# Kernel optimization log

Hardware: AMD Instinct MI355X
Metric: run time of the kernel (lower is better)

## Reference

```python
import jax, jax.numpy as jnp
import numpy as np

N_V, N_G, K, C_IN, DW, NB, E = 8192, 4096, 128, 128, 64, 4, 65536
SIGMA, CUT = 4.0, 8.0


def setup_inputs() -> dict:
    key = jax.random.key(0)
    ks = iter(jax.random.split(key, 64))
    s = 0.05
    def rn(shape):
        return jax.random.normal(next(ks), shape, dtype=jnp.float32) * s
    p = {}
    p['vertices'] = jax.random.uniform(next(ks), (N_V, 3), dtype=jnp.float32) * 30.0
    p['graph_pos'] = jax.random.uniform(next(ks), (N_G, 3), dtype=jnp.float32) * 30.0
    p['x_in'] = jax.random.normal(next(ks), (N_V, C_IN), dtype=jnp.float32)
    p['graph_x'] = jax.random.normal(next(ks), (N_G, C_IN), dtype=jnp.float32)
    p['mass'] = jax.random.uniform(next(ks), (N_V,), dtype=jnp.float32) + 0.5
    p['evals'] = jax.random.uniform(next(ks), (K,), dtype=jnp.float32) * 10.0
    p['evecs'] = jax.random.normal(next(ks), (N_V, K), dtype=jnp.float32) * 0.011
    p['gradX'] = jax.random.normal(next(ks), (N_V, N_V), dtype=jnp.float32) * 0.01
    p['gradY'] = jax.random.normal(next(ks), (N_V, N_V), dtype=jnp.float32) * 0.01
    p['graph_edge_index'] = jax.random.randint(next(ks), (2, E), 0, N_G)
    p['graph_edge_weight'] = jax.random.uniform(next(ks), (E,), dtype=jnp.float32)
    p['lin1_w'] = rn((C_IN, DW)); p['lin1_b'] = rn((DW,))
    p['lin2_w'] = rn((C_IN, DW)); p['lin2_b'] = rn((DW,))
    p['diff_time'] = jax.random.uniform(next(ks), (NB, DW), dtype=jnp.float32) * 0.5 + 0.01
    p['A_re'] = rn((NB, DW, DW)); p['A_im'] = rn((NB, DW, DW))
    p['mlp_w0'] = rn((NB, 3 * DW, DW)); p['mlp_b0'] = rn((NB, DW))
    p['mlp_w1'] = rn((NB, DW, DW)); p['mlp_b1'] = rn((NB, DW))
    p['mlp_w2'] = rn((NB, DW, DW)); p['mlp_b2'] = rn((NB, DW))
    p['gcn1_w'] = rn((NB, DW, DW)); p['gcn1_b'] = rn((NB, DW))
    p['gcn2_w'] = rn((NB, DW, DW)); p['gcn2_b'] = rn((NB, DW))
    p['gs_w'] = rn((NB, DW, DW)); p['gs_b'] = rn((NB, DW))
    p['sg_w'] = rn((NB, DW, DW)); p['sg_b'] = rn((NB, DW))
    return p


def _gcn_conv(x, src, dst, ew, W, b, n):
    # PyG GCNConv with self-loops (fill 1.0): D^-1/2 (A+I) D^-1/2 (x W) + b
    xw = x @ W
    deg = jnp.ones((n,), xw.dtype).at[dst].add(ew)
    dinv = 1.0 / jnp.sqrt(deg)
    norm = dinv[src] * ew * dinv[dst]
    agg = jnp.zeros_like(xw).at[dst].add(norm[:, None] * xw[src])
    return agg + xw / deg[:, None] + b


def _forward(vertices, graph_pos, x_in, graph_x, mass, evals, evecs, gradX, gradY,
             graph_edge_weight, lin1_w, lin1_b, lin2_w, lin2_b, diff_time, A_re, A_im,
             mlp_w0, mlp_b0, mlp_w1, mlp_b1, mlp_w2, mlp_b2,
             gcn1_w, gcn1_b, gcn2_w, gcn2_b, gs_w, gs_b, sg_w, sg_b, graph_edge_index):
    n_v = vertices.shape[0]
    # torch.cdist + cutoff + exp(-d/sigma), under no_grad in the original
    d = jnp.sqrt(jnp.maximum(jnp.sum((vertices[:, None, :] - graph_pos[None, :, :]) ** 2, -1), 0.0))
    Wb = jax.lax.stop_gradient(jnp.where(d < CUT, jnp.exp(-d / SIGMA), 0.0))  # [n_v, n_g]
    deg_v = 1.0 + Wb.sum(1)  # vertex in-degree incl. self-loop (graphsurf direction)
    deg_g = 1.0 + Wb.sum(0)  # graph-node in-degree incl. self-loop (surfgraph direction)
    rsv = 1.0 / jnp.sqrt(deg_v)
    rsg = 1.0 / jnp.sqrt(deg_g)
    src, dst = graph_edge_index[0], graph_edge_index[1]
    diff_x = x_in @ lin1_w + lin1_b
    gx = graph_x @ lin2_w + lin2_b
    n_g = gx.shape[0]
    for i in range(NB):
        # --- DiffusionNet block (spectral) ---
        t = jnp.maximum(diff_time[i], 1e-8)
        spec = evecs.T @ (diff_x * mass[:, None])              # [K, DW]
        xd = evecs @ (jnp.exp(-evals[:, None] * t[None, :]) * spec)
        gX = gradX @ xd                                         # real part of gradient
        gY = gradY @ xd                                         # imag part of gradient
        br = gX @ A_re[i] - gY @ A_im[i]
        bi = gY @ A_re[i] + gX @ A_im[i]
        gf = jnp.tanh(gX * br + gY * bi)                        # spatial gradient features
        h = jnp.concatenate([diff_x, xd, gf], axis=-1)
        h = jax.nn.relu(h @ mlp_w0[i] + mlp_b0[i])
        h = jax.nn.relu(h @ mlp_w1[i] + mlp_b1[i])
        diff_x = diff_x + h @ mlp_w2[i] + mlp_b2[i]
        # --- internal graph GCN (eval mode: dropout = identity) ---
        gx = jax.nn.relu(_gcn_conv(gx, src, dst, graph_edge_weight, gcn1_w[i], gcn1_b[i], n_g))
        gx = _gcn_conv(gx, src, dst, graph_edge_weight, gcn2_w[i], gcn2_b[i], n_g)
        # --- bipartite GCNConvs on concatenated nodes ---
        xall = jnp.concatenate([diff_x, gx], axis=0)
        xw = xall @ gs_w[i]   # graphsurf: graph -> surface edges
        os_v = xw[:n_v] / deg_v[:, None] + (Wb @ xw[n_v:]) * rsv[:, None] + gs_b[i]
        os_g = xw[n_v:] + gs_b[i]
        xw2 = xall @ sg_w[i]  # surfgraph: surface -> graph edges
        og_g = xw2[n_v:] / deg_g[:, None] + (Wb.T @ xw2[:n_v]) * rsg[:, None] + sg_b[i]
        og_v = xw2[:n_v] + sg_b[i]
        diff_x = 0.5 * (os_v + og_v)
        gx = 0.5 * (os_g + og_g)
    return diff_x  # [n_v, C_out]


def reference(vertices, graph_pos, x_in, graph_x, mass, evals, evecs, gradX, gradY,
              graph_edge_index, graph_edge_weight, lin1_w, lin1_b, lin2_w, lin2_b,
              diff_time, A_re, A_im, mlp_w0, mlp_b0, mlp_w1, mlp_b1, mlp_w2, mlp_b2,
              gcn1_w, gcn1_b, gcn2_w, gcn2_b, gs_w, gs_b, sg_w, sg_b):
    return _forward(vertices, graph_pos, x_in, graph_x, mass, evals, evecs, gradX, gradY,
                    graph_edge_weight, lin1_w, lin1_b, lin2_w, lin2_b, diff_time, A_re, A_im,
                    mlp_w0, mlp_b0, mlp_w1, mlp_b1, mlp_w2, mlp_b2,
                    gcn1_w, gcn1_b, gcn2_w, gcn2_b, gs_w, gs_b, sg_w, sg_b, graph_edge_index)
```

## Files before the change

kernel.cpp:

```cpp
#include <hip/hip_runtime.h>
#include <hip/hip_bf16.h>

typedef unsigned short u16;
typedef __attribute__((ext_vector_type(8))) short sh8;
typedef __attribute__((ext_vector_type(4))) float f32x4;

#define NV 8192
#define NG 4096
#define NE 65536
#define NSLICE 32

__device__ __forceinline__ u16 f2bf(float f) {
  __hip_bfloat16 h = __float2bfloat16(f);
  return __builtin_bit_cast(u16, h);
}

__device__ __forceinline__ void gl_lds16(const void* g, void* l) {
  __builtin_amdgcn_global_load_lds(
      (const __attribute__((address_space(1))) void*)g,
      (__attribute__((address_space(3))) void*)l, 16, 0, 0);
}

__global__ void k_fill4(float* __restrict__ deg_v, float* __restrict__ deg_g,
                        float* __restrict__ deg_e, int* __restrict__ cnt) {
  int i = blockIdx.x * 256 + threadIdx.x;
  if (i < NV) deg_v[i] = 1.f;
  int j = i - NV;
  if (j >= 0 && j < NG) deg_g[j] = 1.f;
  j -= NG;
  if (j >= 0 && j < NG) deg_e[j] = 1.f;
  j -= NG;
  if (j >= 0 && j < NG) cnt[j] = 0;
}

__global__ __launch_bounds__(256) void k_wb_build(
    const float* __restrict__ vert, const float* __restrict__ gpos,
    u16* __restrict__ Wb, u16* __restrict__ WbT,
    float* __restrict__ deg_v, float* __restrict__ deg_g) {
  __shared__ float lv[192], lg[192], colp[256];
  __shared__ float tile[64][65];
  int t = threadIdx.x;
  int v0 = blockIdx.x * 64, g0 = blockIdx.y * 64;
  if (t < 192) { lv[t] = vert[(size_t)v0 * 3 + t]; lg[t] = gpos[(size_t)g0 * 3 + t]; }
  __syncthreads();
  int w = t >> 6, lane = t & 63;
  float gx_ = lg[lane * 3], gy_ = lg[lane * 3 + 1], gz_ = lg[lane * 3 + 2];
  float csum = 0.f;
  #pragma unroll 4
  for (int s = 0; s < 16; s++) {
    int vl = w + 4 * s;
    float dx = lv[vl * 3] - gx_, dy = lv[vl * 3 + 1] - gy_, dz = lv[vl * 3 + 2] - gz_;
    float d = sqrtf(dx * dx + dy * dy + dz * dz);
    float W = (d < 8.0f) ? expf(d * -0.25f) : 0.f;
    Wb[(size_t)(v0 + vl) * NG + g0 + lane] = f2bf(W);
    tile[vl][lane] = W;
    csum += W;
  }
  colp[t] = csum;
  __syncthreads();
  int r = t >> 2, q = t & 3;
  float rs = 0.f;
  #pragma unroll
  for (int j = 0; j < 16; j++) rs += tile[r][q * 16 + j];
  rs += __shfl_xor(rs, 1);
  rs += __shfl_xor(rs, 2);
  if (q == 0) atomicAdd(&deg_v[v0 + r], rs);
  if (w == 0) {
    float tot = colp[lane] + colp[64 + lane] + colp[128 + lane] + colp[192 + lane];
    atomicAdd(&deg_g[g0 + lane], tot);
  }
  if (WbT != nullptr) {
    #pragma unroll
    for (int j = 0; j < 2; j++) {
      int idx = j * 256 + t;
      int g = idx >> 3, v8 = (idx & 7) * 8;
      u16 pk[8];
      #pragma unroll
      for (int qq = 0; qq < 8; qq++) pk[qq] = f2bf(tile[v8 + qq][g]);
      *(uint4*)&WbT[(size_t)(g0 + g) * NV + v0 + v8] = *(uint4*)pk;
    }
  }
}

__global__ void k_recips(const float* __restrict__ deg_v, float* __restrict__ inv_v,
                         float* __restrict__ rs_v, const float* __restrict__ deg_g,
                         float* __restrict__ inv_g, float* __restrict__ rs_g,
                         const float* __restrict__ deg_e, float* __restrict__ inv_e,
                         float* __restrict__ rs_e) {
  int i = blockIdx.x * 256 + threadIdx.x;
  if (i < NV) { float d = deg_v[i]; inv_v[i] = 1.f / d; rs_v[i] = 1.f / sqrtf(d); }
  else if (i < NV + NG) {
    int j = i - NV; float d = deg_g[j]; inv_g[j] = 1.f / d; rs_g[j] = 1.f / sqrtf(d);
  } else if (i < NV + 2 * NG) {
    int j = i - NV - NG; float d = deg_e[j]; inv_e[j] = 1.f / d; rs_e[j] = 1.f / sqrtf(d);
  }
}

__global__ void k_edge_prep(const int* __restrict__ eidx, const float* __restrict__ ew,
                            float* __restrict__ deg_e, int* __restrict__ cnt) {
  int e = blockIdx.x * 256 + threadIdx.x;
  if (e < NE) { int d = eidx[NE + e]; atomicAdd(&deg_e[d], ew[e]); atomicAdd(&cnt[d], 1); }
}

__global__ __launch_bounds__(1024) void k_scan(const int* __restrict__ cnt,
    int* __restrict__ row_ptr, int* __restrict__ cursor) {
  __shared__ int buf0[1024], buf1[1024];
  int t = threadIdx.x;
  int b = t * 4;
  int c0 = cnt[b], c1 = cnt[b + 1], c2 = cnt[b + 2], c3 = cnt[b + 3];
  int s = c0 + c1 + c2 + c3;
  buf0[t] = s;
  __syncthreads();
  int* src = buf0; int* dst = buf1;
  for (int off = 1; off < 1024; off <<= 1) {
    int v = src[t];
    if (t >= off) v += src[t - off];
    dst[t] = v;
    __syncthreads();
    int* tmp = src; src = dst; dst = tmp;
  }
  int excl = (t == 0) ? 0 : src[t - 1];
  int r0 = excl, r1 = excl + c0, r2 = excl + c0 + c1, r3 = excl + c0 + c1 + c2;
  row_ptr[b] = r0; row_ptr[b + 1] = r1; row_ptr[b + 2] = r2; row_ptr[b + 3] = r3;
  cursor[b] = r0; cursor[b + 1] = r1; cursor[b + 2] = r2; cursor[b + 3] = r3;
  if (t == 1023) row_ptr[4096] = src[1023];
}

__global__ void k_scatter(const int* __restrict__ eidx, const float* __restrict__ ew,
                          const float* __restrict__ dinv, int* __restrict__ cursor,
                          int* __restrict__ csrc, float* __restrict__ cnorm) {
  int e = blockIdx.x * 256 + threadIdx.x;
  if (e < NE) {
    int s = eidx[e], d = eidx[NE + e];
    int slot = atomicAdd(&cursor[d], 1);
    csrc[slot] = s;
    cnorm[slot] = dinv[s] * ew[e] * dinv[d];
  }
}

__global__ __launch_bounds__(256) void k_evecsT(const float* __restrict__ ev, u16* __restrict__ evT) {
  __shared__ float tile[32][33];
  int t = threadIdx.x;
  int v0 = blockIdx.x * 32, k0 = blockIdx.y * 32;
  int r = t >> 3, c4 = (t & 7) * 4;
  float4 x = *(const float4*)(ev + (size_t)(v0 + r) * 128 + k0 + c4);
  tile[r][c4] = x.x; tile[r][c4 + 1] = x.y; tile[r][c4 + 2] = x.z; tile[r][c4 + 3] = x.w;
  __syncthreads();
  u16* dst = evT + (size_t)(k0 + r) * NV + v0 + c4;
  dst[0] = f2bf(tile[c4][r]); dst[1] = f2bf(tile[c4 + 1][r]);
  dst[2] = f2bf(tile[c4 + 2][r]); dst[3] = f2bf(tile[c4 + 3][r]);
}

__global__ __launch_bounds__(256) void gemm_setup(
    const float* __restrict__ gXm, const float* __restrict__ gYm,
    const u16* __restrict__ evT, float* __restrict__ parts,
    int nzHalf, int kchunk) {
  __shared__ __align__(16) char smem[49152];
  const int t = threadIdx.x;
  const int lane = t & 63, wave = t >> 6;
  const int m0 = blockIdx.x * 128;
  int kz = blockIdx.z;
  const float* A = gXm;
  if (kz >= nzHalf) { A = gYm; kz -= nzHalf; }
  const int kbeg = kz * kchunk;
  const int nt = kchunk >> 5;
  const int wm = (wave >> 1) * 64, wn = (wave & 1) * 64;
  const int arl = lane >> 3, asl = lane & 7;
  const int brl = lane >> 2, bsl = lane & 3;

  f32x4 acc[4][4];
  #pragma unroll
  for (int a = 0; a < 4; a++)
    #pragma unroll
    for (int b = 0; b < 4; b++) acc[a][b] = f32x4{0.f, 0.f, 0.f, 0.f};

  auto STAGE = [&](int buf, int k0) {
    char* base = smem + buf * 24576;
    #pragma unroll
    for (int j = 0; j < 4; j++) {
      int R0 = (wave * 4 + j) * 8;
      int r = R0 + arl;
      int gs = asl ^ (r & 7);
      gl_lds16(A + (size_t)(m0 + r) * NV + k0 + gs * 4, base + R0 * 128);
    }
    char* bb = base + 16384;
    #pragma unroll
    for (int j = 0; j < 2; j++) {
      int R0 = (wave * 2 + j) * 16;
      int r = R0 + brl;
      int gs = bsl ^ (r & 3);
      gl_lds16(evT + (size_t)r * NV + k0 + gs * 8, bb + R0 * 64);
    }
  };

  auto COMPUTE = [&](int buf) {
    char* base = smem + buf * 24576;
    const float* Af = (const float*)base;
    const u16* Bf = (const u16*)(base + 16384);
    sh8 av[4], bv[4];
    #pragma unroll
    for (int mf = 0; mf < 4; mf++) {
      int r = wm + mf * 16 + (lane & 15);
      int b2 = (lane >> 4) * 2;
      float4 f0 = *(const float4*)(Af + r * 32 + ((b2) ^ (r & 7)) * 4);
      float4 f1 = *(const float4*)(Af + r * 32 + ((b2 + 1) ^ (r & 7)) * 4);
      sh8 v;
      v[0] = (short)f2bf(f0.x); v[1] = (short)f2bf(f0.y);
      v[2] = (short)f2bf(f0.z); v[3] = (short)f2bf(f0.w);
      v[4] = (short)f2bf(f1.x); v[5] = (short)f2bf(f1.y);
      v[6] = (short)f2bf(f1.z); v[7] = (short)f2bf(f1.w);
      av[mf] = v;
    }
    #pragma unroll
    for (int nf = 0; nf < 4; nf++) {
      int r = wn + nf * 16 + (lane & 15);
      int s = (lane >> 4) ^ (r & 3);
      bv[nf] = *(const sh8*)(Bf + r * 32 + s * 8);
    }
    #pragma unroll
    for (int mf = 0; mf < 4; mf++)
      #pragma unroll
      for (int nf = 0; nf < 4; nf++)
        acc[mf][nf] = __builtin_amdgcn_mfma_f32_16x16x32_bf16(av[mf], bv[nf], acc[mf][nf], 0, 0, 0);
  };

  STAGE(0, kbeg);
  if (nt > 1) STAGE(1, kbeg + 32);
  for (int ti = 0; ti < nt; ti++) {
    if (ti + 1 < nt) { asm volatile("s_waitcnt vmcnt(6)" ::: "memory"); }
    else             { asm volatile("s_waitcnt vmcnt(0)" ::: "memory"); }
    __builtin_amdgcn_sched_barrier(0);
    __builtin_amdgcn_s_barrier();
    COMPUTE(ti & 1);
    __builtin_amdgcn_sched_barrier(0);
    __builtin_amdgcn_s_barrier();
    if (ti + 2 < nt) STAGE(ti & 1, kbeg + (ti + 2) * 32);
  }

  float* C = parts + (size_t)blockIdx.z * (NV * 128);
  #pragma unroll
  for (int mf = 0; mf < 4; mf++)
    #pragma unroll
    for (int nf = 0; nf < 4; nf++) {
      int row = m0 + wm + mf * 16 + (lane >> 4) * 4;
      int col = wn + nf * 16 + (lane & 15);
      #pragma unroll
      for (int q = 0; q < 4; q++)
        C[(size_t)(row + q) * 128 + col] = acc[mf][nf][q];
    }
}

__global__ __launch_bounds__(256) void gemm_bf16(
    const u16* __restrict__ Ab, int lda, const u16* __restrict__ BT, int ldbt,
    float* __restrict__ parts, int M, int kchunk) {
  __shared__ __align__(16) char smem[49152];
  const int t = threadIdx.x;
  const int lane = t & 63, wave = t >> 6;
  const int m0 = blockIdx.x * 128;
  const int kbeg = blockIdx.z * kchunk;
  const int nt = kchunk >> 6;
  const int wm = (wave >> 1) * 64, wn = (wave & 1) * 32;
  const int arl = lane >> 3, asl = lane & 7;

  f32x4 acc[4][2];
  #pragma unroll
  for (int a = 0; a < 4; a++)
    #pragma unroll
    for (int b = 0; b < 2; b++) acc[a][b] = f32x4{0.f, 0.f, 0.f, 0.f};

  auto STAGE = [&](int buf, int k0) {
    char* base = smem + buf * 24576;
    #pragma unroll
    for (int j = 0; j < 4; j++) {
      int R0 = (wave * 4 + j) * 8;
      int r = R0 + arl;
      int gs = asl ^ (r & 7);
      gl_lds16(Ab + (size_t)(m0 + r) * lda + k0 + gs * 8, base + R0 * 128);
    }
    char* bb = base + 16384;
    #pragma unroll
    for (int j = 0; j < 2; j++) {
      int R0 = (wave * 2 + j) * 8;
      int r = R0 + arl;
      int gs = asl ^ (r & 7);
      gl_lds16(BT + (size_t)r * ldbt + k0 + gs * 8, bb + R0 * 128);
    }
  };

  auto COMPUTE = [&](int buf) {
    char* base = smem + buf * 24576;
    const u16* Af = (const u16*)base;
    const u16* Bf = (const u16*)(base + 16384);
    #pragma unroll
    for (int kk = 0; kk < 2; kk++) {
      sh8 av[4], bv[2];
      #pragma unroll
      for (int mf = 0; mf < 4; mf++) {
        int r = wm + mf * 16 + (lane & 15);
        int g = kk * 4 + (lane >> 4);
        av[mf] = *(const sh8*)(Af + r * 64 + (g ^ (r & 7)) * 8);
      }
      #pragma unroll
      for (int nf = 0; nf < 2; nf++) {
        int r = wn + nf * 16 + (lane & 15);
        int g = kk * 4 + (lane >> 4);
        bv[nf] = *(const sh8*)(Bf + r * 64 + (g ^ (r & 7)) * 8);
      }
      #pragma unroll
      for (int mf = 0; mf < 4; mf++)
        #pragma unroll
        for (int nf = 0; nf < 2; nf++)
          acc[mf][nf] = __builtin_amdgcn_mfma_f32_16x16x32_bf16(av[mf], bv[nf], acc[mf][nf], 0, 0, 0);
    }
  };

  STAGE(0, kbeg);
  if (nt > 1) STAGE(1, kbeg + 64);
  for (int ti = 0; ti < nt; ti++) {
    if (ti + 1 < nt) { asm volatile("s_waitcnt vmcnt(6)" ::: "memory"); }
    else             { asm volatile("s_waitcnt vmcnt(0)" ::: "memory"); }
    __builtin_amdgcn_sched_barrier(0);
    __builtin_amdgcn_s_barrier();
    COMPUTE(ti & 1);
    __builtin_amdgcn_sched_barrier(0);
    __builtin_amdgcn_s_barrier();
    if (ti + 2 < nt) STAGE(ti & 1, kbeg + (ti + 2) * 64);
  }

  float* C = parts + (size_t)blockIdx.z * M * 64;
  #pragma unroll
  for (int mf = 0; mf < 4; mf++)
    #pragma unroll
    for (int nf = 0; nf < 2; nf++) {
      int row = m0 + wm + mf * 16 + (lane >> 4) * 4;
      int col = wn + nf * 16 + (lane & 15);
      #pragma unroll
      for (int q = 0; q < 4; q++)
        C[(size_t)(row + q) * 64 + col] = acc[mf][nf][q];
    }
}

template<int BN, bool AF32, bool ATRANS>
__global__ __launch_bounds__(256) void gemm_k(
    const void* __restrict__ Aptr, const void* __restrict__ A2, int zsplit2,
    const u16* __restrict__ BT, float* __restrict__ Cpart,
    int M, int N, int lda, int ldbt, int kchunk) {
  constexpr int NF = BN / 32;
  __shared__ u16 lA[128 * 40];
  __shared__ u16 lB[BN * 40];
  const int t = threadIdx.x;
  const int m0 = blockIdx.x * 128, n0 = blockIdx.y * BN;
  const void* Ause = Aptr;
  int kz = blockIdx.z;
  if (A2 != nullptr && kz >= zsplit2) { Ause = A2; kz -= zsplit2; }
  const int kbeg = kz * kchunk;
  const int lane = t & 63, wave = t >> 6;
  const int wm = (wave >> 1) * 64, wn = (wave & 1) * (BN / 2);
  f32x4 zero = {0.f, 0.f, 0.f, 0.f};
  f32x4 acc[4][NF];
  #pragma unroll
  for (int a = 0; a < 4; a++)
    #pragma unroll
    for (int b = 0; b < NF; b++) acc[a][b] = zero;

  for (int k0 = kbeg; k0 < kbeg + kchunk; k0 += 32) {
    if constexpr (!ATRANS) {
      const int r = t >> 1, cc = (t & 1) * 16;
      const u16* A = (const u16*)Ause + (size_t)(m0 + r) * lda + k0 + cc;
      *(uint4*)&lA[r * 40 + cc] = *(const uint4*)A;
      *(uint4*)&lA[r * 40 + cc + 8] = *(const uint4*)(A + 8);
    } else {
      const int kl = t >> 3, mb = (t & 7) * 16;
      const u16* A = (const u16*)Ause + (size_t)(k0 + kl) * lda + m0 + mb;
      u16 vals[16];
      *(uint4*)&vals[0] = *(const uint4*)A;
      *(uint4*)&vals[8] = *(const uint4*)(A + 8);
      #pragma unroll
      for (int j = 0; j < 16; j++) lA[(mb + j) * 40 + kl] = vals[j];
    }
    if constexpr (BN == 64) {
      const int r = t >> 2, cc = (t & 3) * 8;
      const u16* B = BT + (size_t)(n0 + r) * ldbt + k0 + cc;
      *(uint4*)&lB[r * 40 + cc] = *(const uint4*)B;
    } else {
      const int r = t >> 1, cc = (t & 1) * 16;
      const u16* B = BT + (size_t)(n0 + r) * ldbt + k0 + cc;
      *(uint4*)&lB[r * 40 + cc] = *(const uint4*)B;
      *(uint4*)&lB[r * 40 + cc + 8] = *(const uint4*)(B + 8);
    }
    __syncthreads();
    sh8 af[4], bfv[NF];
    #pragma unroll
    for (int mf = 0; mf < 4; mf++)
      af[mf] = *(const sh8*)&lA[(wm + mf * 16 + (lane & 15)) * 40 + (lane >> 4) * 8];
    #pragma unroll
    for (int nf = 0; nf < NF; nf++)
      bfv[nf] = *(const sh8*)&lB[(wn + nf * 16 + (lane & 15)) * 40 + (lane >> 4) * 8];
    #pragma unroll
    for (int mf = 0; mf < 4; mf++)
      #pragma unroll
      for (int nf = 0; nf < NF; nf++)
        acc[mf][nf] = __builtin_amdgcn_mfma_f32_16x16x32_bf16(af[mf], bfv[nf], acc[mf][nf], 0, 0, 0);
    __syncthreads();
  }
  float* C = Cpart + (size_t)blockIdx.z * M * N;
  #pragma unroll
  for (int mf = 0; mf < 4; mf++)
    #pragma unroll
    for (int nf = 0; nf < NF; nf++) {
      const int row = m0 + wm + mf * 16 + (lane >> 4) * 4;
      const int col = n0 + wn + nf * 16 + (lane & 15);
      #pragma unroll
      for (int q = 0; q < 4; q++)
        C[(size_t)(row + q) * N + col] = acc[mf][nf][q];
    }
}

__global__ void k_reduce(const float* __restrict__ parts, float* __restrict__ dst, int len, int nz) {
  int i = (blockIdx.x * 256 + threadIdx.x) * 4;
  if (i >= len) return;
  float4 s = *(const float4*)(parts + i);
  for (int z = 1; z < nz; z++) {
    float4 v = *(const float4*)(parts + (size_t)z * len + i);
    s.x += v.x; s.y += v.y; s.z += v.z; s.w += v.w;
  }
  *(float4*)(dst + i) = s;
}

__global__ void k_reduce2(const float* __restrict__ parts, float* __restrict__ dst, int len, int nz) {
  int i = (blockIdx.x * 256 + threadIdx.x) * 4;
  if (i >= 2 * len) return;
  int mat = i / len, j = i - mat * len;
  const float* src = parts + (size_t)mat * nz * len + j;
  float4 s = *(const float4*)src;
  for (int z = 1; z < nz; z++) {
    float4 v = *(const float4*)(src + (size_t)z * len);
    s.x += v.x; s.y += v.y; s.z += v.z; s.w += v.w;
  }
  *(float4*)(dst + i) = s;
}

__global__ __launch_bounds__(256) void k_lin_both(const float* __restrict__ x_in,
    const float* __restrict__ graph_x, const float* __restrict__ W1,
    const float* __restrict__ b1, const float* __restrict__ W2,
    const float* __restrict__ b2, float* __restrict__ outV, float* __restrict__ outG) {
  __shared__ float lW[8192];
  __shared__ float lb[64];
  int bb = blockIdx.x;
  bool isV = bb < 2048;
  const float* W = isV ? W1 : W2;
  const float* bi = isV ? b1 : b2;
  const float* A = isV ? x_in : graph_x;
  float* out = isV ? outV : outG;
  int rb = isV ? bb : bb - 2048;
  int t = threadIdx.x;
  for (int i = t; i < 8192; i += 256) lW[i] = W[i];
  if (t < 64) lb[t] = bi[t];
  __syncthreads();
  int row = rb * 4 + (t >> 6), c = t & 63;
  const float* Ar = A + (size_t)row * 128;
  float acc = lb[c];
  #pragma unroll 8
  for (int k = 0; k < 128; k++) acc += Ar[k] * lW[k * 64 + c];
  out[(size_t)row * 64 + c] = acc;
}

__global__ __launch_bounds__(64) void k_spec_part(const float* __restrict__ evecs,
    const float* __restrict__ mass, const float* __restrict__ dx, float* __restrict__ sp) {
  int k = blockIdx.x, c = threadIdx.x;
  int v0 = blockIdx.y * 256;
  float a0 = 0, a1 = 0, a2 = 0, a3 = 0;
  for (int v = v0; v < v0 + 256; v += 4) {
    a0 += evecs[(size_t)(v + 0) * 128 + k] * mass[v + 0] * dx[(size_t)(v + 0) * 64 + c];
    a1 += evecs[(size_t)(v + 1) * 128 + k] * mass[v + 1] * dx[(size_t)(v + 1) * 64 + c];
    a2 += evecs[(size_t)(v + 2) * 128 + k] * mass[v + 2] * dx[(size_t)(v + 2) * 64 + c];
    a3 += evecs[(size_t)(v + 3) * 128 + k] * mass[v + 3] * dx[(size_t)(v + 3) * 64 + c];
  }
  sp[(size_t)blockIdx.y * 8192 + k * 64 + c] = (a0 + a1) + (a2 + a3);
}

__global__ void k_es(const float* __restrict__ sp, const float* __restrict__ evals,
                     const float* __restrict__ dt, float* __restrict__ Es) {
  int i = blockIdx.x * 256 + threadIdx.x;
  int k = i >> 6, c = i & 63;
  float s = 0.f;
  #pragma unroll 8
  for (int z = 0; z < NSLICE; z++) s += sp[(size_t)z * 8192 + i];
  Es[i] = expf(-evals[k] * fmaxf(dt[c], 1e-8f)) * s;
}

__global__ __launch_bounds__(256) void k_xdgf(const float* __restrict__ evecs,
    const float* __restrict__ GXE, const float* __restrict__ GYE,
    const float* __restrict__ Es, const float* __restrict__ Are,
    const float* __restrict__ Aim, float* __restrict__ xd, float* __restrict__ gf) {
  __shared__ float lE[8192];
  __shared__ float lr[4096], li[4096];
  __shared__ float lgx[256], lgy[256];
  int t = threadIdx.x;
  for (int i = t; i < 8192; i += 256) lE[i] = Es[i];
  for (int i = t; i < 4096; i += 256) { lr[i] = Are[i]; li[i] = Aim[i]; }
  __syncthreads();
  int wr = t >> 6, c = t & 63;
  int row = blockIdx.x * 4 + wr;
  const float* er = evecs + (size_t)row * 128;
  const float* xr = GXE + (size_t)row * 128;
  const float* yr = GYE + (size_t)row * 128;
  float a0 = 0, a1 = 0, a2 = 0;
  #pragma unroll 8
  for (int k = 0; k < 128; k++) {
    float s = lE[k * 64 + c];
    a0 += er[k] * s; a1 += xr[k] * s; a2 += yr[k] * s;
  }
  lgx[wr * 64 + c] = a1;
  lgy[wr * 64 + c] = a2;
  __syncthreads();
  float br = 0.f, bi = 0.f;
  #pragma unroll 8
  for (int k = 0; k < 64; k++) {
    float gx = lgx[wr * 64 + k], gy = lgy[wr * 64 + k];
    float ar = lr[k * 64 + c], ai = li[k * 64 + c];
    br += gx * ar - gy * ai;
    bi += gy * ar + gx * ai;
  }
  xd[(size_t)row * 64 + c] = a0;
  gf[(size_t)row * 64 + c] = tanhf(a1 * br + a2 * bi);
}

__global__ __launch_bounds__(256) void k_mlp0(const float* __restrict__ dx,
    const float* __restrict__ xd, const float* __restrict__ gf,
    const float* __restrict__ W0, const float* __restrict__ b0, float* __restrict__ h1) {
  __shared__ float lW[12288];
  __shared__ float lb[64];
  int t = threadIdx.x;
  for (int i = t; i < 12288; i += 256) lW[i] = W0[i];
  if (t < 64) lb[t] = b0[t];
  __syncthreads();
  int row = blockIdx.x * 4 + (t >> 6), c = t & 63;
  const float* a0 = dx + (size_t)row * 64;
  const float* a1 = xd + (size_t)row * 64;
  const float* a2 = gf + (size_t)row * 64;
  float acc = lb[c];
  #pragma unroll 8
  for (int k = 0; k < 64; k++) acc += a0[k] * lW[k * 64 + c];
  #pragma unroll 8
  for (int k = 0; k < 64; k++) acc += a1[k] * lW[(64 + k) * 64 + c];
  #pragma unroll 8
  for (int k = 0; k < 64; k++) acc += a2[k] * lW[(128 + k) * 64 + c];
  h1[(size_t)row * 64 + c] = fmaxf(acc, 0.f);
}

__global__ __launch_bounds__(256) void k_mlp12(const float* __restrict__ h1,
    const float* __restrict__ W1, const float* __restrict__ b1,
    const float* __restrict__ W2, const float* __restrict__ b2, float* __restrict__ dx) {
  __shared__ float l1[4096], l2[4096], lb1[64], lb2[64], lrow[256];
  int t = threadIdx.x;
  for (int i = t; i < 4096; i += 256) { l1[i] = W1[i]; l2[i] = W2[i]; }
  if (t < 64) lb1[t] = b1[t];
  else if (t < 128) lb2[t - 64] = b2[t - 64];
  __syncthreads();
  int wr = t >> 6, c = t & 63;
  int row = blockIdx.x * 4 + wr;
  const float* hr = h1 + (size_t)row * 64;
  float h2 = lb1[c];
  #pragma unroll 8
  for (int k = 0; k < 64; k++) h2 += hr[k] * l1[k * 64 + c];
  h2 = fmaxf(h2, 0.f);
  lrow[wr * 64 + c] = h2;
  __syncthreads();
  float o = lb2[c] + dx[(size_t)row * 64 + c];
  #pragma unroll 8
  for (int k = 0; k < 64; k++) o += lrow[wr * 64 + k] * l2[k * 64 + c];
  dx[(size_t)row * 64 + c] = o;
}

template<bool BIAS, bool RELU, bool RES>
__global__ __launch_bounds__(256) void k_mm64(const float* __restrict__ A,
    const float* __restrict__ W, const float* __restrict__ b,
    const float* __restrict__ res, float* __restrict__ out) {
  __shared__ float lW[4096];
  __shared__ float lb[64];
  int t = threadIdx.x;
  for (int i = t; i < 4096; i += 256) lW[i] = W[i];
  if constexpr (BIAS) { if (t < 64) lb[t] = b[t]; }
  __syncthreads();
  int row = blockIdx.x * 4 + (t >> 6), c = t & 63;
  const float* Ar = A + (size_t)row * 64;
  float acc = 0.f;
  #pragma unroll 8
  for (int k = 0; k < 64; k++) acc += Ar[k] * lW[k * 64 + c];
  if constexpr (BIAS) acc += lb[c];
  if constexpr (RES) acc += res[(size_t)row * 64 + c];
  if constexpr (RELU) acc = fmaxf(acc, 0.f);
  out[(size_t)row * 64 + c] = acc;
}

template<bool TP, bool TQ>
__global__ __launch_bounds__(256) void k_mm_dual(const float* __restrict__ A,
    const float* __restrict__ W1, const float* __restrict__ W2,
    float* __restrict__ P, float* __restrict__ Q,
    u16* __restrict__ PT, u16* __restrict__ QT, int R) {
  __shared__ float l1[4096], l2[4096];
  int t = threadIdx.x;
  for (int i = t; i < 4096; i += 256) { l1[i] = W1[i]; l2[i] = W2[i]; }
  __syncthreads();
  int row = blockIdx.x * 4 + (t >> 6), c = t & 63;
  const float* Ar = A + (size_t)row * 64;
  float p = 0.f, q = 0.f;
  #pragma unroll 8
  for (int k = 0; k < 64; k++) { float a = Ar[k]; p += a * l1[k * 64 + c]; q += a * l2[k * 64 + c]; }
  P[(size_t)row * 64 + c] = p;
  Q[(size_t)row * 64 + c] = q;
  if constexpr (TP) PT[(size_t)c * R + row] = f2bf(p);
  if constexpr (TQ) QT[(size_t)c * R + row] = f2bf(q);
}

__global__ __launch_bounds__(64) void k_aggmm(const float* __restrict__ xw,
    const int* __restrict__ rp, const int* __restrict__ csrc,
    const float* __restrict__ cnorm, const float* __restrict__ invdeg,
    const float* __restrict__ b1, const float* __restrict__ W2, float* __restrict__ out) {
  __shared__ float lrow[64];
  int g = blockIdx.x, c = threadIdx.x;
  float acc = xw[(size_t)g * 64 + c] * invdeg[g] + b1[c];
  int j1 = rp[g + 1];
  for (int j = rp[g]; j < j1; j++) acc += cnorm[j] * xw[(size_t)csrc[j] * 64 + c];
  acc = fmaxf(acc, 0.f);
  lrow[c] = acc;
  __syncthreads();
  float o = 0.f;
  #pragma unroll 8
  for (int k = 0; k < 64; k++) o += lrow[k] * W2[k * 64 + c];
  out[(size_t)g * 64 + c] = o;
}

__global__ __launch_bounds__(64) void k_aggdual(const float* __restrict__ xw,
    const int* __restrict__ rp, const int* __restrict__ csrc,
    const float* __restrict__ cnorm, const float* __restrict__ invdeg,
    const float* __restrict__ b2, const float* __restrict__ gsw,
    const float* __restrict__ sgw, float* __restrict__ xw_g,
    float* __restrict__ xw2_g, u16* __restrict__ xwgT) {
  __shared__ float lrow[64];
  int g = blockIdx.x, c = threadIdx.x;
  float acc = xw[(size_t)g * 64 + c] * invdeg[g] + b2[c];
  int j1 = rp[g + 1];
  for (int j = rp[g]; j < j1; j++) acc += cnorm[j] * xw[(size_t)csrc[j] * 64 + c];
  lrow[c] = acc;
  __syncthreads();
  float p = 0.f, q = 0.f;
  #pragma unroll 8
  for (int k = 0; k < 64; k++) {
    float r = lrow[k];
    p += r * gsw[k * 64 + c];
    q += r * sgw[k * 64 + c];
  }
  xw_g[(size_t)g * 64 + c] = p;
  xw2_g[(size_t)g * 64 + c] = q;
  xwgT[(size_t)c * NG + g] = f2bf(p);
}

__global__ void k_combine(const float* __restrict__ xw_v, const float* __restrict__ Wbp,
    const float* __restrict__ xw2_v, const float* __restrict__ xw_g,
    const float* __restrict__ WbTp, const float* __restrict__ xw2_g,
    const float* __restrict__ inv_deg_v, const float* __restrict__ rsv,
    const float* __restrict__ inv_deg_g, const float* __restrict__ rsg,
    const float* __restrict__ gsb, const float* __restrict__ sgb,
    float* __restrict__ dx, float* __restrict__ gx) {
  int idx = blockIdx.x * 256 + threadIdx.x;
  if (idx < NV * 64) {
    int v = idx >> 6, c = idx & 63;
    dx[idx] = 0.5f * (xw_v[idx] * inv_deg_v[v] + Wbp[idx] * rsv[v] + gsb[c] + xw2_v[idx] + sgb[c]);
  } else {
    int j = idx - NV * 64;
    int g = j >> 6, c = j & 63;
    gx[j] = 0.5f * (xw_g[j] + gsb[c] + xw2_g[j] * inv_deg_g[g] + WbTp[j] * rsg[g] + sgb[c]);
  }
}

extern "C" void kernel_launch(void* const* d_in, const int* in_sizes, int n_in,
                              void* d_out, int out_size, void* d_ws, size_t ws_size,
                              hipStream_t stream) {
  const float* vertices  = (const float*)d_in[0];
  const float* graph_pos = (const float*)d_in[1];
  const float* x_in      = (const float*)d_in[2];
  const float* graph_x   = (const float*)d_in[3];
  const float* mass      = (const float*)d_in[4];
  const float* evals     = (const float*)d_in[5];
  const float* evecs     = (const float*)d_in[6];
  const float* gradX     = (const float*)d_in[7];
  const float* gradY     = (const float*)d_in[8];
  const int*   eidx      = (const int*)d_in[9];
  const float* ew        = (const float*)d_in[10];
  const float* lin1_w    = (const float*)d_in[11];
  const float* lin1_b    = (const float*)d_in[12];
  const float* lin2_w    = (const float*)d_in[13];
  const float* lin2_b    = (const float*)d_in[14];
  const float* diff_time = (const float*)d_in[15];
  const float* A_re      = (const float*)d_in[16];
  const float* A_im      = (const float*)d_in[17];
  const float* mlp_w0    = (const float*)d_in[18];
  const float* mlp_b0    = (const float*)d_in[19];
  const float* mlp_w1    = (const float*)d_in[20];
  const float* mlp_b1    = (const float*)d_in[21];
  const float* mlp_w2    = (const float*)d_in[22];
  const float* mlp_b2    = (const float*)d_in[23];
  const float* gcn1_w    = (const float*)d_in[24];
  const float* gcn1_b    = (const float*)d_in[25];
  const float* gcn2_w    = (const float*)d_in[26];
  const float* gcn2_b    = (const float*)d_in[27];
  const float* gs_w      = (const float*)d_in[28];
  const float* gs_b      = (const float*)d_in[29];
  const float* sg_w      = (const float*)d_in[30];
  const float* sg_b      = (const float*)d_in[31];

  char* base = (char*)d_ws;
  size_t off = 0;
  auto alloc = [&](size_t nbytes) -> void* {
    void* p = base + off;
    off += (nbytes + 255) & ~(size_t)255;
    return p;
  };
  const size_t MBy = 1024 * 1024;
  u16*   Wb_bf   = (u16*)alloc((size_t)NV * NG * 2);
  u16*   evecsT  = (u16*)alloc((size_t)128 * NV * 2);
  float* GXE2    = (float*)alloc((size_t)2 * NV * 128 * 4);
  float* GXE     = GXE2;
  float* GYE     = GXE2 + (size_t)NV * 128;
  float* sp      = (float*)alloc((size_t)NSLICE * 8192 * 4);
  float* Es      = (float*)alloc(8192 * 4);
  float* diffx   = (float*)alloc((size_t)NV * 64 * 4);
  float* gxb     = (float*)alloc((size_t)NG * 64 * 4);
  float* xd      = (float*)alloc((size_t)NV * 64 * 4);
  float* gf      = (float*)alloc((size_t)NV * 64 * 4);
  float* h1      = (float*)alloc((size_t)NV * 64 * 4);
  float* xw_v    = (float*)alloc((size_t)NV * 64 * 4);
  float* xw2_v   = (float*)alloc((size_t)NV * 64 * 4);
  float* xw_g    = (float*)alloc((size_t)NG * 64 * 4);
  float* xw2_g   = (float*)alloc((size_t)NG * 64 * 4);
  float* xw1     = (float*)alloc((size_t)NG * 64 * 4);
  float* xw2k    = (float*)alloc((size_t)NG * 64 * 4);
  u16*   xwgT    = (u16*)alloc((size_t)64 * NG * 2);
  u16*   xw2vT   = (u16*)alloc((size_t)64 * NV * 2);
  float* Wbp     = (float*)alloc((size_t)NV * 64 * 4);
  float* WbTp    = (float*)alloc((size_t)NG * 64 * 4);
  float* deg_v   = (float*)alloc(NV * 4);
  float* inv_deg_v = (float*)alloc(NV * 4);
  float* rsv     = (float*)alloc(NV * 4);
  float* deg_g   = (float*)alloc(NG * 4);
  float* inv_deg_g = (float*)alloc(NG * 4);
  float* rsg     = (float*)alloc(NG * 4);
  float* deg_e   = (float*)alloc(NG * 4);
  float* invdeg_e = (float*)alloc(NG * 4);
  float* dinv_e  = (float*)alloc(NG * 4);
  int*   cnt     = (int*)alloc(NG * 4);
  int*   row_ptr = (int*)alloc((NG + 1) * 4);
  int*   cursor  = (int*)alloc(NG * 4);
  int*   csr_src = (int*)alloc(NE * 4);
  float* csr_norm = (float*)alloc(NE * 4);

  size_t avail = ws_size > off ? ws_size - off : 0;
  u16* WbT_bf = nullptr;
  int nzHalf;
  size_t partsBytes;
  if (avail >= 129 * MBy)      { WbT_bf = (u16*)alloc((size_t)NG * NV * 2); partsBytes = 64 * MBy; nzHalf = 8; }
  else if (avail >= 97 * MBy)  { WbT_bf = (u16*)alloc((size_t)NG * NV * 2); partsBytes = 32 * MBy; nzHalf = 4; }
  else if (avail >= 81 * MBy)  { WbT_bf = (u16*)alloc((size_t)NG * NV * 2); partsBytes = 16 * MBy; nzHalf = 2; }
  else if (avail >= 33 * MBy)  { partsBytes = 32 * MBy; nzHalf = 4; }
  else                          { partsBytes = 16 * MBy; nzHalf = 2; }
  float* parts = (float*)alloc(partsBytes);
  if (off > ws_size) return;

  dim3 B256(256);

  k_fill4<<<dim3(80), B256, 0, stream>>>(deg_v, deg_g, deg_e, cnt);
  k_wb_build<<<dim3(128, 64), B256, 0, stream>>>(vertices, graph_pos, Wb_bf, WbT_bf, deg_v, deg_g);
  k_edge_prep<<<dim3(256), B256, 0, stream>>>(eidx, ew, deg_e, cnt);
  k_recips<<<dim3(64), B256, 0, stream>>>(deg_v, inv_deg_v, rsv, deg_g, inv_deg_g, rsg,
                                          deg_e, invdeg_e, dinv_e);
  k_scan<<<dim3(1), dim3(1024), 0, stream>>>(cnt, row_ptr, cursor);
  k_scatter<<<dim3(256), B256, 0, stream>>>(eidx, ew, dinv_e, cursor, csr_src, csr_norm);
  k_evecsT<<<dim3(256, 4), B256, 0, stream>>>(evecs, evecsT);
  gemm_setup<<<dim3(64, 1, 2 * nzHalf), B256, 0, stream>>>(
      gradX, gradY, evecsT, parts, nzHalf, 8192 / nzHalf);
  k_reduce2<<<dim3(2048), B256, 0, stream>>>(parts, GXE2, NV * 128, nzHalf);
  k_lin_both<<<dim3(3072), B256, 0, stream>>>(x_in, graph_x, lin1_w, lin1_b, lin2_w, lin2_b, diffx, gxb);

  for (int i = 0; i < 4; i++) {
    const float* dtrow = diff_time + i * 64;
    k_spec_part<<<dim3(128, NSLICE), dim3(64), 0, stream>>>(evecs, mass, diffx, sp);
    k_es<<<dim3(32), B256, 0, stream>>>(sp, evals, dtrow, Es);
    k_xdgf<<<dim3(2048), B256, 0, stream>>>(evecs, GXE, GYE, Es, A_re + i * 4096, A_im + i * 4096, xd, gf);
    k_mlp0<<<dim3(2048), B256, 0, stream>>>(diffx, xd, gf, mlp_w0 + i * 12288, mlp_b0 + i * 64, h1);
    k_mlp12<<<dim3(2048), B256, 0, stream>>>(h1, mlp_w1 + i * 4096, mlp_b1 + i * 64,
        mlp_w2 + i * 4096, mlp_b2 + i * 64, diffx);
    k_mm64<false, false, false><<<dim3(1024), B256, 0, stream>>>(gxb, gcn1_w + i * 4096, nullptr, nullptr, xw1);
    k_aggmm<<<dim3(NG), dim3(64), 0, stream>>>(xw1, row_ptr, csr_src, csr_norm, invdeg_e,
        gcn1_b + i * 64, gcn2_w + i * 4096, xw2k);
    k_aggdual<<<dim3(NG), dim3(64), 0, stream>>>(xw2k, row_ptr, csr_src, csr_norm, invdeg_e,
        gcn2_b + i * 64, gs_w + i * 4096, sg_w + i * 4096, xw_g, xw2_g, xwgT);
    k_mm_dual<false, true><<<dim3(2048), B256, 0, stream>>>(diffx, gs_w + i * 4096, sg_w + i * 4096,
        xw_v, xw2_v, nullptr, xw2vT, NV);
    gemm_bf16<<<dim3(64, 1, 8), B256, 0, stream>>>(
        Wb_bf, NG, xwgT, NG, parts, NV, 512);
    k_reduce<<<dim3(512), B256, 0, stream>>>(parts, Wbp, NV * 64, 8);
    if (WbT_bf != nullptr) {
      gemm_bf16<<<dim3(32, 1, 16), B256, 0, stream>>>(
          WbT_bf, NV, xw2vT, NV, parts, NG, 512);
    } else {
      gemm_k<64, false, true><<<dim3(32, 1, 16), B256, 0, stream>>>(
          Wb_bf, nullptr, 1 << 30, xw2vT, parts, NG, 64, NG, NV, 512);
    }
    k_reduce<<<dim3(256), B256, 0, stream>>>(parts, WbTp, NG * 64, 16);
    k_combine<<<dim3(3072), B256, 0, stream>>>(xw_v, Wbp, xw2_v, xw_g, WbTp, xw2_g,
        inv_deg_v, rsv, inv_deg_g, rsg, gs_b + i * 64, sg_b + i * 64, diffx, gxb);
  }

  hipMemcpyAsync(d_out, diffx, (size_t)NV * 64 * 4, hipMemcpyDeviceToDevice, stream);
}
```

Before: 1.152 ms.

## Store Wb in pre-swizzled tile panels and replace split-K setup GEMM

The kernel that builds Wb now writes it, and its transpose, as contiguous pre-swizzled 128x64 bf16 tiles. A new gemm_panel kernel streams each tile straight into LDS with fully contiguous loads, replacing the strided row-major loads in the per-block Wb GEMMs. The setup gradX/gradY times evecs GEMM is rewritten without split-K: 64-row blocks with a 128-wide K stage and 128KB of dynamic LDS write directly to the output, which removes the partials buffer and the k_reduce2 pass. The cost is a workspace requirement of about 146MB for the fast path, and the setup GEMM now runs with fewer blocks and higher LDS use per block, which can lower occupancy.

```diff
diff --git a/kernel.cpp b/kernel.cpp
--- a/kernel.cpp
+++ b/kernel.cpp
@@ -35,7 +35,7 @@
 
 __global__ __launch_bounds__(256) void k_wb_build(
     const float* __restrict__ vert, const float* __restrict__ gpos,
-    u16* __restrict__ Wb, u16* __restrict__ WbT,
+    u16* __restrict__ WbRow, u16* __restrict__ WbP, u16* __restrict__ WbTP,
     float* __restrict__ deg_v, float* __restrict__ deg_g) {
   __shared__ float lv[192], lg[192], colp[256];
   __shared__ float tile[64][65];
@@ -52,32 +52,47 @@
     float dx = lv[vl * 3] - gx_, dy = lv[vl * 3 + 1] - gy_, dz = lv[vl * 3 + 2] - gz_;
     float d = sqrtf(dx * dx + dy * dy + dz * dz);
     float W = (d < 8.0f) ? expf(d * -0.25f) : 0.f;
-    Wb[(size_t)(v0 + vl) * NG + g0 + lane] = f2bf(W);
+    if (WbRow != nullptr) WbRow[(size_t)(v0 + vl) * NG + g0 + lane] = f2bf(W);
     tile[vl][lane] = W;
     csum += W;
   }
   colp[t] = csum;
   __syncthreads();
-  int r = t >> 2, q = t & 3;
+  int r4 = t >> 2, q = t & 3;
   float rs = 0.f;
   #pragma unroll
-  for (int j = 0; j < 16; j++) rs += tile[r][q * 16 + j];
+  for (int j = 0; j < 16; j++) rs += tile[r4][q * 16 + j];
   rs += __shfl_xor(rs, 1);
   rs += __shfl_xor(rs, 2);
-  if (q == 0) atomicAdd(&deg_v[v0 + r], rs);
+  if (q == 0) atomicAdd(&deg_v[v0 + r4], rs);
   if (w == 0) {
     float tot = colp[lane] + colp[64 + lane] + colp[128 + lane] + colp[192 + lane];
     atomicAdd(&deg_g[g0 + lane], tot);
   }
-  if (WbT != nullptr) {
+  if (WbP != nullptr) {
+    size_t tb = ((size_t)(v0 >> 7) * 64 + (g0 >> 6)) * 8192;
     #pragma unroll
     for (int j = 0; j < 2; j++) {
       int idx = j * 256 + t;
-      int g = idx >> 3, v8 = (idx & 7) * 8;
+      int vr = idx >> 3, k8 = (idx & 7) * 8;
       u16 pk[8];
       #pragma unroll
-      for (int qq = 0; qq < 8; qq++) pk[qq] = f2bf(tile[v8 + qq][g]);
-      *(uint4*)&WbT[(size_t)(g0 + g) * NV + v0 + v8] = *(uint4*)pk;
+      for (int qq = 0; qq < 8; qq++) pk[qq] = f2bf(tile[vr][k8 + qq]);
+      int r = (v0 & 64) + vr;
+      *(uint4*)&WbP[tb + (size_t)r * 64 + (size_t)(((k8 >> 3) ^ (r & 7)) << 3)] = *(uint4*)pk;
+    }
+  }
+  if (WbTP != nullptr) {
+    size_t tb = ((size_t)(g0 >> 7) * 128 + (v0 >> 6)) * 8192;
+    #pragma unroll
+    for (int j = 0; j < 2; j++) {
+      int idx = j * 256 + t;
+      int gr = idx >> 3, v8 = (idx & 7) * 8;
+      u16 pk[8];
+      #pragma unroll
+      for (int qq = 0; qq < 8; qq++) pk[qq] = f2bf(tile[v8 + qq][gr]);
+      int r = (g0 & 64) + gr;
+      *(uint4*)&WbTP[tb + (size_t)r * 64 + (size_t)(((v8 >> 3) ^ (r & 7)) << 3)] = *(uint4*)pk;
     }
   }
 }
@@ -151,102 +166,185 @@
   dst[2] = f2bf(tile[c4 + 2][r]); dst[3] = f2bf(tile[c4 + 3][r]);
 }
 
-__global__ __launch_bounds__(256) void gemm_setup(
+__global__ __launch_bounds__(256) void gemm_setup2(
     const float* __restrict__ gXm, const float* __restrict__ gYm,
-    const u16* __restrict__ evT, float* __restrict__ parts,
-    int nzHalf, int kchunk) {
-  __shared__ __align__(16) char smem[49152];
+    const u16* __restrict__ evT, float* __restrict__ C2) {
+  extern __shared__ __align__(16) char smem[];
   const int t = threadIdx.x;
   const int lane = t & 63, wave = t >> 6;
-  const int m0 = blockIdx.x * 128;
-  int kz = blockIdx.z;
-  const float* A = gXm;
-  if (kz >= nzHalf) { A = gYm; kz -= nzHalf; }
-  const int kbeg = kz * kchunk;
-  const int nt = kchunk >> 5;
-  const int wm = (wave >> 1) * 64, wn = (wave & 1) * 64;
-  const int arl = lane >> 3, asl = lane & 7;
-  const int brl = lane >> 2, bsl = lane & 3;
-
-  f32x4 acc[4][4];
+  const int rl = lane & 15, hi = lane >> 4;
+  const int mat = blockIdx.x >> 7, mb = blockIdx.x & 127;
+  const int m0 = mb * 64;
+  const float* A = mat ? gYm : gXm;
+  const int wm = (wave >> 1) * 32, wn = (wave & 1) * 64;
+
+  f32x4 acc[2][4];
   #pragma unroll
-  for (int a = 0; a < 4; a++)
+  for (int a = 0; a < 2; a++)
     #pragma unroll
     for (int b = 0; b < 4; b++) acc[a][b] = f32x4{0.f, 0.f, 0.f, 0.f};
 
   auto STAGE = [&](int buf, int k0) {
-    char* base = smem + buf * 24576;
-    #pragma unroll
-    for (int j = 0; j < 4; j++) {
-      int R0 = (wave * 4 + j) * 8;
-      int r = R0 + arl;
-      int gs = asl ^ (r & 7);
-      gl_lds16(A + (size_t)(m0 + r) * NV + k0 + gs * 4, base + R0 * 128);
-    }
-    char* bb = base + 16384;
-    #pragma unroll
-    for (int j = 0; j < 2; j++) {
-      int R0 = (wave * 2 + j) * 16;
-      int r = R0 + brl;
-      int gs = bsl ^ (r & 3);
-      gl_lds16(evT + (size_t)r * NV + k0 + gs * 8, bb + R0 * 64);
+    char* aB = smem + buf * 65536;
+    #pragma unroll
+    for (int jj = 0; jj < 8; jj++) {
+      int j = wave * 8 + jj;
+      int r = 2 * j + (lane >> 5);
+      const float* src = A + (size_t)(m0 + r) * NV + k0 + (((lane & 31) ^ (r & 7)) << 2);
+      gl_lds16(src, aB + j * 1024);
+    }
+    char* bB = aB + 32768;
+    #pragma unroll
+    for (int jj = 0; jj < 8; jj++) {
+      int j = wave * 8 + jj;
+      int n = 4 * j + (lane >> 4);
+      const u16* srcb = evT + (size_t)n * NV + k0 + (((lane & 15) ^ (n & 7)) << 3);
+      gl_lds16(srcb, bB + j * 1024);
     }
   };
 
   auto COMPUTE = [&](int buf) {
-    char* base = smem + buf * 24576;
-    const float* Af = (const float*)base;
-    const u16* Bf = (const u16*)(base + 16384);
-    sh8 av[4], bv[4];
-    #pragma unroll
-    for (int mf = 0; mf < 4; mf++) {
-      int r = wm + mf * 16 + (lane & 15);
-      int b2 = (lane >> 4) * 2;
-      float4 f0 = *(const float4*)(Af + r * 32 + ((b2) ^ (r & 7)) * 4);
-      float4 f1 = *(const float4*)(Af + r * 32 + ((b2 + 1) ^ (r & 7)) * 4);
-      sh8 v;
-      v[0] = (short)f2bf(f0.x); v[1] = (short)f2bf(f0.y);
-      v[2] = (short)f2bf(f0.z); v[3] = (short)f2bf(f0.w);
-      v[4] = (short)f2bf(f1.x); v[5] = (short)f2bf(f1.y);
-      v[6] = (short)f2bf(f1.z); v[7] = (short)f2bf(f1.w);
-      av[mf] = v;
-    }
-    #pragma unroll
-    for (int nf = 0; nf < 4; nf++) {
-      int r = wn + nf * 16 + (lane & 15);
-      int s = (lane >> 4) ^ (r & 3);
-      bv[nf] = *(const sh8*)(Bf + r * 32 + s * 8);
-    }
-    #pragma unroll
-    for (int mf = 0; mf < 4; mf++)
-      #pragma unroll
-      for (int nf = 0; nf < 4; nf++)
-        acc[mf][nf] = __builtin_amdgcn_mfma_f32_16x16x32_bf16(av[mf], bv[nf], acc[mf][nf], 0, 0, 0);
+    const float* Af = (const float*)(smem + buf * 65536);
+    const u16* Bf = (const u16*)(smem + buf * 65536 + 32768);
+    #pragma unroll
+    for (int step = 0; step < 4; step++) {
+      sh8 av[2], bv[4];
+      #pragma unroll
+      for (int mf = 0; mf < 2; mf++) {
+        int r = wm + mf * 16 + rl;
+        int s0 = step * 8 + hi * 2;
+        f32x4 lo = *(const f32x4*)(Af + r * 128 + ((s0 ^ (r & 7)) << 2));
+        f32x4 hi4 = *(const f32x4*)(Af + r * 128 + (((s0 + 1) ^ (r & 7)) << 2));
+        sh8 v;
+        v[0] = (short)f2bf(lo[0]); v[1] = (short)f2bf(lo[1]);
+        v[2] = (short)f2bf(lo[2]); v[3] = (short)f2bf(lo[3]);
+        v[4] = (short)f2bf(hi4[0]); v[5] = (short)f2bf(hi4[1]);
+        v[6] = (short)f2bf(hi4[2]); v[7] = (short)f2bf(hi4[3]);
+        av[mf] = v;
+      }
+      #pragma unroll
+      for (int nf = 0; nf < 4; nf++) {
+        int n = wn + nf * 16 + rl;
+        int s = step * 4 + hi;
+        bv[nf] = *(const sh8*)(Bf + n * 128 + ((s ^ (n & 7)) << 3));
+      }
+      #pragma unroll
+      for (int mf = 0; mf < 2; mf++)
+        #pragma unroll
+        for (int nf = 0; nf < 4; nf++)
+          acc[mf][nf] = __builtin_amdgcn_mfma_f32_16x16x32_bf16(av[mf], bv[nf], acc[mf][nf], 0, 0, 0);
+    }
   };
 
-  STAGE(0, kbeg);
-  if (nt > 1) STAGE(1, kbeg + 32);
-  for (int ti = 0; ti < nt; ti++) {
-    if (ti + 1 < nt) { asm volatile("s_waitcnt vmcnt(6)" ::: "memory"); }
+  STAGE(0, 0);
+  STAGE(1, 128);
+  for (int ti = 0; ti < 64; ti++) {
+    if (ti + 1 < 64) { asm volatile("s_waitcnt vmcnt(16)" ::: "memory"); }
     else             { asm volatile("s_waitcnt vmcnt(0)" ::: "memory"); }
     __builtin_amdgcn_sched_barrier(0);
     __builtin_amdgcn_s_barrier();
     COMPUTE(ti & 1);
     __builtin_amdgcn_sched_barrier(0);
     __builtin_amdgcn_s_barrier();
-    if (ti + 2 < nt) STAGE(ti & 1, kbeg + (ti + 2) * 32);
-  }
-
-  float* C = parts + (size_t)blockIdx.z * (NV * 128);
+    if (ti + 2 < 64) STAGE(ti & 1, (ti + 2) * 128);
+  }
+
+  float* C = C2 + (size_t)mat * NV * 128;
   #pragma unroll
-  for (int mf = 0; mf < 4; mf++)
+  for (int mf = 0; mf < 2; mf++)
     #pragma unroll
     for (int nf = 0; nf < 4; nf++) {
-      int row = m0 + wm + mf * 16 + (lane >> 4) * 4;
-      int col = wn + nf * 16 + (lane & 15);
+      int row = m0 + wm + mf * 16 + hi * 4;
+      int col = wn + nf * 16 + rl;
       #pragma unroll
       for (int q = 0; q < 4; q++)
         C[(size_t)(row + q) * 128 + col] = acc[mf][nf][q];
+    }
+}
+
+__global__ __launch_bounds__(256) void gemm_panel(
+    const u16* __restrict__ Apan, int KT, const u16* __restrict__ BT, int ldbt,
+    float* __restrict__ parts, int M, int nz, int ktpz) {
+  __shared__ __align__(16) char smem[49152];
+  const int t = threadIdx.x;
+  const int lane = t & 63, wave = t >> 6;
+  const int rl = lane & 15, hi = lane >> 4;
+  const int mb = blockIdx.x / nz, z = blockIdx.x % nz;
+  const int kt0 = z * ktpz;
+  const int wm = wave * 32;
+
+  f32x4 acc[2][4];
+  #pragma unroll
+  for (int a = 0; a < 2; a++)
+    #pragma unroll
+    for (int b = 0; b < 4; b++) acc[a][b] = f32x4{0.f, 0.f, 0.f, 0.f};
+
+  auto STAGE = [&](int buf, int kt) {
+    char* aB = smem + buf * 24576;
+    const u16* tbase = Apan + ((size_t)mb * KT + kt) * 8192;
+    #pragma unroll
+    for (int jj = 0; jj < 4; jj++) {
+      int j = wave * 4 + jj;
+      gl_lds16(tbase + j * 512 + lane * 8, aB + j * 1024);
+    }
+    char* bB = aB + 16384;
+    #pragma unroll
+    for (int jj = 0; jj < 2; jj++) {
+      int j = wave * 2 + jj;
+      int n = 8 * j + (lane >> 3);
+      const u16* srcb = BT + (size_t)n * ldbt + kt * 64 + (((lane & 7) ^ (n & 7)) << 3);
+      gl_lds16(srcb, bB + j * 1024);
+    }
+  };
+
+  auto COMPUTE = [&](int buf) {
+    const u16* Af = (const u16*)(smem + buf * 24576);
+    const u16* Bf = Af + 8192;
+    #pragma unroll
+    for (int step = 0; step < 2; step++) {
+      sh8 av[2], bv[4];
+      int s = step * 4 + hi;
+      #pragma unroll
+      for (int mf = 0; mf < 2; mf++) {
+        int r = wm + mf * 16 + rl;
+        av[mf] = *(const sh8*)(Af + r * 64 + ((s ^ (r & 7)) << 3));
+      }
+      #pragma unroll
+      for (int nf = 0; nf < 4; nf++) {
+        int n = nf * 16 + rl;
+        bv[nf] = *(const sh8*)(Bf + n * 64 + ((s ^ (n & 7)) << 3));
+      }
+      #pragma unroll
+      for (int mf = 0; mf < 2; mf++)
+        #pragma unroll
+        for (int nf = 0; nf < 4; nf++)
+          acc[mf][nf] = __builtin_amdgcn_mfma_f32_16x16x32_bf16(av[mf], bv[nf], acc[mf][nf], 0, 0, 0);
+    }
+  };
+
+  STAGE(0, kt0);
+  if (ktpz > 1) STAGE(1, kt0 + 1);
+  for (int ti = 0; ti < ktpz; ti++) {
+    if (ti + 1 < ktpz) { asm volatile("s_waitcnt vmcnt(6)" ::: "memory"); }
+    else               { asm volatile("s_waitcnt vmcnt(0)" ::: "memory"); }
+    __builtin_amdgcn_sched_barrier(0);
+    __builtin_amdgcn_s_barrier();
+    COMPUTE(ti & 1);
+    __builtin_amdgcn_sched_barrier(0);
+    __builtin_amdgcn_s_barrier();
+    if (ti + 2 < ktpz) STAGE(ti & 1, kt0 + ti + 2);
+  }
+
+  float* C = parts + (size_t)z * M * 64;
+  #pragma unroll
+  for (int mf = 0; mf < 2; mf++)
+    #pragma unroll
+    for (int nf = 0; nf < 4; nf++) {
+      int row = mb * 128 + wm + mf * 16 + hi * 4;
+      int col = nf * 16 + rl;
+      #pragma unroll
+      for (int q = 0; q < 4; q++)
+        C[(size_t)(row + q) * 64 + col] = acc[mf][nf][q];
     }
 }
 
@@ -422,19 +520,6 @@
   float4 s = *(const float4*)(parts + i);
   for (int z = 1; z < nz; z++) {
     float4 v = *(const float4*)(parts + (size_t)z * len + i);
-    s.x += v.x; s.y += v.y; s.z += v.z; s.w += v.w;
-  }
-  *(float4*)(dst + i) = s;
-}
-
-__global__ void k_reduce2(const float* __restrict__ parts, float* __restrict__ dst, int len, int nz) {
-  int i = (blockIdx.x * 256 + threadIdx.x) * 4;
-  if (i >= 2 * len) return;
-  int mat = i / len, j = i - mat * len;
-  const float* src = parts + (size_t)mat * nz * len + j;
-  float4 s = *(const float4*)src;
-  for (int z = 1; z < nz; z++) {
-    float4 v = *(const float4*)(src + (size_t)z * len);
     s.x += v.x; s.y += v.y; s.z += v.z; s.w += v.w;
   }
   *(float4*)(dst + i) = s;
@@ -719,7 +804,6 @@
     return p;
   };
   const size_t MBy = 1024 * 1024;
-  u16*   Wb_bf   = (u16*)alloc((size_t)NV * NG * 2);
   u16*   evecsT  = (u16*)alloc((size_t)128 * NV * 2);
   float* GXE2    = (float*)alloc((size_t)2 * NV * 128 * 4);
   float* GXE     = GXE2;
@@ -757,30 +841,32 @@
   float* csr_norm = (float*)alloc(NE * 4);
 
   size_t avail = ws_size > off ? ws_size - off : 0;
-  u16* WbT_bf = nullptr;
-  int nzHalf;
-  size_t partsBytes;
-  if (avail >= 129 * MBy)      { WbT_bf = (u16*)alloc((size_t)NG * NV * 2); partsBytes = 64 * MBy; nzHalf = 8; }
-  else if (avail >= 97 * MBy)  { WbT_bf = (u16*)alloc((size_t)NG * NV * 2); partsBytes = 32 * MBy; nzHalf = 4; }
-  else if (avail >= 81 * MBy)  { WbT_bf = (u16*)alloc((size_t)NG * NV * 2); partsBytes = 16 * MBy; nzHalf = 2; }
-  else if (avail >= 33 * MBy)  { partsBytes = 32 * MBy; nzHalf = 4; }
-  else                          { partsBytes = 16 * MBy; nzHalf = 2; }
-  float* parts = (float*)alloc(partsBytes);
+  u16 *WbP = nullptr, *WbTP = nullptr, *WbRow = nullptr;
+  float* parts;
+  if (avail >= 146 * MBy) {
+    WbP  = (u16*)alloc((size_t)NV * NG * 2);
+    WbTP = (u16*)alloc((size_t)NG * NV * 2);
+    parts = (float*)alloc(16 * MBy);
+  } else if (avail >= 81 * MBy) {
+    WbRow = (u16*)alloc((size_t)NV * NG * 2);
+    parts = (float*)alloc(16 * MBy);
+  } else {
+    WbRow = (u16*)alloc((size_t)NV * NG * 2);
+    parts = (float*)alloc(16 * MBy);
+  }
   if (off > ws_size) return;
 
   dim3 B256(256);
 
   k_fill4<<<dim3(80), B256, 0, stream>>>(deg_v, deg_g, deg_e, cnt);
-  k_wb_build<<<dim3(128, 64), B256, 0, stream>>>(vertices, graph_pos, Wb_bf, WbT_bf, deg_v, deg_g);
+  k_wb_build<<<dim3(128, 64), B256, 0, stream>>>(vertices, graph_pos, WbRow, WbP, WbTP, deg_v, deg_g);
   k_edge_prep<<<dim3(256), B256, 0, stream>>>(eidx, ew, deg_e, cnt);
   k_recips<<<dim3(64), B256, 0, stream>>>(deg_v, inv_deg_v, rsv, deg_g, inv_deg_g, rsg,
                                           deg_e, invdeg_e, dinv_e);
   k_scan<<<dim3(1), dim3(1024), 0, stream>>>(cnt, row_ptr, cursor);
   k_scatter<<<dim3(256), B256, 0, stream>>>(eidx, ew, dinv_e, cursor, csr_src, csr_norm);
   k_evecsT<<<dim3(256, 4), B256, 0, stream>>>(evecs, evecsT);
-  gemm_setup<<<dim3(64, 1, 2 * nzHalf), B256, 0, stream>>>(
-      gradX, gradY, evecsT, parts, nzHalf, 8192 / nzHalf);
-  k_reduce2<<<dim3(2048), B256, 0, stream>>>(parts, GXE2, NV * 128, nzHalf);
+  gemm_setup2<<<dim3(256), B256, 131072, stream>>>(gradX, gradY, evecsT, GXE2);
   k_lin_both<<<dim3(3072), B256, 0, stream>>>(x_in, graph_x, lin1_w, lin1_b, lin2_w, lin2_b, diffx, gxb);
 
   for (int i = 0; i < 4; i++) {
@@ -798,17 +884,18 @@
         gcn2_b + i * 64, gs_w + i * 4096, sg_w + i * 4096, xw_g, xw2_g, xwgT);
     k_mm_dual<false, true><<<dim3(2048), B256, 0, stream>>>(diffx, gs_w + i * 4096, sg_w + i * 4096,
         xw_v, xw2_v, nullptr, xw2vT, NV);
-    gemm_bf16<<<dim3(64, 1, 8), B256, 0, stream>>>(
-        Wb_bf, NG, xwgT, NG, parts, NV, 512);
-    k_reduce<<<dim3(512), B256, 0, stream>>>(parts, Wbp, NV * 64, 8);
-    if (WbT_bf != nullptr) {
-      gemm_bf16<<<dim3(32, 1, 16), B256, 0, stream>>>(
-          WbT_bf, NV, xw2vT, NV, parts, NG, 512);
+    if (WbP != nullptr) {
+      gemm_panel<<<dim3(64 * 8), B256, 0, stream>>>(WbP, 64, xwgT, NG, parts, NV, 8, 8);
+      k_reduce<<<dim3(512), B256, 0, stream>>>(parts, Wbp, NV * 64, 8);
+      gemm_panel<<<dim3(32 * 16), B256, 0, stream>>>(WbTP, 128, xw2vT, NV, parts, NG, 16, 8);
+      k_reduce<<<dim3(256), B256, 0, stream>>>(parts, WbTp, NG * 64, 16);
     } else {
+      gemm_bf16<<<dim3(64, 1, 8), B256, 0, stream>>>(WbRow, NG, xwgT, NG, parts, NV, 512);
+      k_reduce<<<dim3(512), B256, 0, stream>>>(parts, Wbp, NV * 64, 8);
       gemm_k<64, false, true><<<dim3(32, 1, 16), B256, 0, stream>>>(
-          Wb_bf, nullptr, 1 << 30, xw2vT, parts, NG, 64, NG, NV, 512);
-    }
-    k_reduce<<<dim3(256), B256, 0, stream>>>(parts, WbTp, NG * 64, 16);
+          WbRow, nullptr, 1 << 30, xw2vT, parts, NG, 64, NG, NV, 512);
+      k_reduce<<<dim3(256), B256, 0, stream>>>(parts, WbTp, NG * 64, 16);
+    }
     k_combine<<<dim3(3072), B256, 0, stream>>>(xw_v, Wbp, xw2_v, xw_g, WbTp, xw2_g,
         inv_deg_v, rsv, inv_deg_g, rsg, gs_b + i * 64, sg_b + i * 64, diffx, gxb);
   }
```

Measured after the change: 1.070 ms. 7.1% less time.
